# Optimization experiments

Measured on AMD Instinct MI355X. Metric: run time of the kernel, lower is better.

## Reference

```python
import jax, jax.numpy as jnp
import numpy as np

EMB = 768
NH = 12
DH = EMB // NH
NORM = float(np.sqrt(DH))  # 8.0


def setup_inputs() -> dict:
    key = jax.random.key(0)
    ks = jax.random.split(key, 9)
    B, S = 1, 4096
    s = 0.02  # realistic init scale for weights
    return {
        "x": jax.random.normal(ks[0], (B, S, EMB), jnp.float32),
        "mask": jnp.ones((B, S), jnp.float32),
        "Wq": jax.random.normal(ks[1], (EMB, EMB), jnp.float32) * s,
        "bq": jnp.zeros((EMB,), jnp.float32),
        "Wk": jax.random.normal(ks[2], (EMB, EMB), jnp.float32) * s,
        "bk": jnp.zeros((EMB,), jnp.float32),
        "Wv": jax.random.normal(ks[3], (EMB, EMB), jnp.float32) * s,
        "bv": jnp.zeros((EMB,), jnp.float32),
        "Wo": jax.random.normal(ks[4], (EMB, EMB), jnp.float32) * s,
        "bo": jnp.zeros((EMB,), jnp.float32),
    }


def reference(x, mask, Wq, bq, Wk, bk, Wv, bv, Wo, bo):
    B, S, _ = x.shape
    # QKV projections (torch Linear: x @ W.T + b)
    q = x @ Wq.T + bq
    k = x @ Wk.T + bk
    v = x @ Wv.T + bv
    # split heads: b s (nh dh) -> b nh s dh
    split = lambda t: t.reshape(B, S, NH, DH).transpose(0, 2, 1, 3)
    qh, kh, vh = split(q), split(k), split(v)
    # attention scores [b, nh, s, s]
    scores = jnp.einsum("bhqd,bhkd->bhqk", qh, kh) / NORM
    # additive mask: scores -= 10000 * (1 - mask), mask broadcast over query dim
    scores = scores - 10000.0 * (1.0 - mask[:, None, None, :])
    attn = jax.nn.softmax(scores, axis=-1)
    out = jnp.einsum("bhqk,bhkd->bhqd", attn, vh)
    # b nh s dh -> b s (nh dh)
    out = out.transpose(0, 2, 1, 3).reshape(B, S, EMB)
    return out @ Wo.T + bo
```

## Files before the change

kernel.cpp:

```cpp
#include <hip/hip_runtime.h>
#include <stdint.h>
#include <stddef.h>

#define EMB 768
#define SEQ 4096
#define NH 12
#define DH 64
#define LOG2E 1.44269504f
#define HALF (SEQ / 2)
#define NBLK (NH * 32 * 2)

typedef __attribute__((ext_vector_type(8))) short short8;
typedef __attribute__((ext_vector_type(2))) float f32x2;
typedef __attribute__((ext_vector_type(4))) float f32x4;
typedef __attribute__((ext_vector_type(8))) float f32x8;
typedef __attribute__((ext_vector_type(16))) float f32x16;
typedef __attribute__((ext_vector_type(2))) unsigned int uint32x2;

static __device__ __forceinline__ unsigned short f2bf(float f) {
  union { float f; uint32_t u; } v; v.f = f;
  uint32_t u = v.u;
  return (unsigned short)((u + 0x7FFFu + ((u >> 16) & 1u)) >> 16);
}

static __device__ __forceinline__ void gl_lds16(const void* g, void* l) {
  __builtin_amdgcn_global_load_lds(
      (const __attribute__((address_space(1))) uint32_t*)g,
      (__attribute__((address_space(3))) uint32_t*)l, 16, 0, 0);
}
static __device__ __forceinline__ void gl_lds4(const void* g, void* l) {
  __builtin_amdgcn_global_load_lds(
      (const __attribute__((address_space(1))) uint32_t*)g,
      (__attribute__((address_space(3))) uint32_t*)l, 4, 0, 0);
}

static __device__ __forceinline__ float xhalf_max(float v) {
  union { float f; unsigned int u; } x; x.f = v;
  uint32x2 r = __builtin_amdgcn_permlane32_swap(x.u, x.u, false, false);
  union { unsigned int u; float f; } a, b; a.u = r[0]; b.u = r[1];
  return fmaxf(a.f, b.f);
}
static __device__ __forceinline__ float xhalf_sum(float v) {
  union { float f; unsigned int u; } x; x.f = v;
  uint32x2 r = __builtin_amdgcn_permlane32_swap(x.u, x.u, false, false);
  union { unsigned int u; float f; } a, b; a.u = r[0]; b.u = r[1];
  return a.f + b.f;
}

static __device__ __forceinline__ f32x8 lo8(f32x16 v) {
  return __builtin_shufflevector(v, v, 0, 1, 2, 3, 4, 5, 6, 7);
}
static __device__ __forceinline__ f32x8 hi8(f32x16 v) {
  return __builtin_shufflevector(v, v, 8, 9, 10, 11, 12, 13, 14, 15);
}
static __device__ __forceinline__ f32x4 lo4(f32x8 v) {
  return __builtin_shufflevector(v, v, 0, 1, 2, 3);
}
static __device__ __forceinline__ f32x4 hi4(f32x8 v) {
  return __builtin_shufflevector(v, v, 4, 5, 6, 7);
}
static __device__ __forceinline__ f32x2 lo2(f32x4 v) {
  return __builtin_shufflevector(v, v, 0, 1);
}
static __device__ __forceinline__ f32x2 hi2(f32x4 v) {
  return __builtin_shufflevector(v, v, 2, 3);
}

__global__ void prep_kernel(const float* __restrict__ x, const float* __restrict__ mask,
                            const float* __restrict__ Wq, const float* __restrict__ Wk,
                            const float* __restrict__ Wv, const float* __restrict__ Wo,
                            unsigned short* __restrict__ xb, unsigned short* __restrict__ wqb,
                            unsigned short* __restrict__ wkb, unsigned short* __restrict__ wvb,
                            unsigned short* __restrict__ wob, float* __restrict__ mb2) {
  const int y = blockIdx.y;
  if (y == 5) {
    int i = blockIdx.x * 256 + threadIdx.x;
    if (i < SEQ) mb2[i] = -80000.f * (1.f - mask[i]);
    return;
  }
  const float* in = y == 0 ? x : y == 1 ? Wq : y == 2 ? Wk : y == 3 ? Wv : Wo;
  unsigned short* out = y == 0 ? xb : y == 1 ? wqb : y == 2 ? wkb : y == 3 ? wvb : wob;
  const int n = (y == 0) ? SEQ * EMB : EMB * EMB;
  int stride = gridDim.x * blockDim.x * 4;
  for (int i = (blockIdx.x * blockDim.x + threadIdx.x) * 4; i < n; i += stride) {
    float4 v = *reinterpret_cast<const float4*>(in + i);
    ushort4 o;
    o.x = f2bf(v.x); o.y = f2bf(v.y); o.z = f2bf(v.z); o.w = f2bf(v.w);
    *reinterpret_cast<ushort4*>(out + i) = o;
  }
}

template <int OUT_F32>
static __device__ __forceinline__ void gemm128(
    const unsigned short* __restrict__ A, const unsigned short* __restrict__ W,
    const float* __restrict__ bias, void* __restrict__ Cout,
    int M, int N, int K, int bm, int bn) {
  __shared__ unsigned short Alds[128 * 64];
  __shared__ unsigned short Blds[128 * 64];
  const int t = threadIdx.x;
  const int lane = t & 63;
  const int wave = t >> 6;
  const int wr = wave >> 1, wc = wave & 1;
  const int lm = lane & 15, lg = lane >> 4;

  f32x4 acc[4][4];
#pragma unroll
  for (int i = 0; i < 4; ++i)
#pragma unroll
    for (int j = 0; j < 4; ++j) acc[i][j] = (f32x4){0.f, 0.f, 0.f, 0.f};

  const int srow = t >> 3;
  const int scsw = (t & 7) * 16;

  const int nK = K >> 6;
  for (int kt = 0; kt < nK; ++kt) {
    const int k0 = kt << 6;
#pragma unroll
    for (int i = 0; i < 4; ++i) {
      int row = i * 32 + srow;
      int cb = scsw ^ ((row & 7) << 4);
      gl_lds16(A + (size_t)(bm * 128 + row) * K + k0 + (cb >> 1),
               (char*)Alds + i * 4096 + t * 16);
      gl_lds16(W + (size_t)(bn * 128 + row) * K + k0 + (cb >> 1),
               (char*)Blds + i * 4096 + t * 16);
    }
    __syncthreads();
#pragma unroll
    for (int kk = 0; kk < 2; ++kk) {
      short8 af[4], bfr[4];
#pragma unroll
      for (int i = 0; i < 4; ++i) {
        int rowa = wr * 64 + i * 16 + lm;
        int cba = (kk * 64 + lg * 16) ^ ((rowa & 7) << 4);
        af[i] = *reinterpret_cast<const short8*>((const char*)Alds + rowa * 128 + cba);
        int rowb = wc * 64 + i * 16 + lm;
        int cbb = (kk * 64 + lg * 16) ^ ((rowb & 7) << 4);
        bfr[i] = *reinterpret_cast<const short8*>((const char*)Blds + rowb * 128 + cbb);
      }
#pragma unroll
      for (int i = 0; i < 4; ++i)
#pragma unroll
        for (int j = 0; j < 4; ++j)
          acc[i][j] = __builtin_amdgcn_mfma_f32_16x16x32_bf16(af[i], bfr[j], acc[i][j], 0, 0, 0);
    }
    __syncthreads();
  }
#pragma unroll
  for (int i = 0; i < 4; ++i) {
    int row0 = bm * 128 + wr * 64 + i * 16 + lg * 4;
#pragma unroll
    for (int j = 0; j < 4; ++j) {
      int col = bn * 128 + wc * 64 + j * 16 + lm;
      float b = bias[col];
#pragma unroll
      for (int r = 0; r < 4; ++r) {
        float v = acc[i][j][r] + b;
        if (OUT_F32)
          ((float*)Cout)[(size_t)(row0 + r) * N + col] = v;
        else
          ((unsigned short*)Cout)[(size_t)(row0 + r) * N + col] = f2bf(v);
      }
    }
  }
}

__global__ __launch_bounds__(256, 2) void gemm_wo(
    const unsigned short* __restrict__ A, const unsigned short* __restrict__ W,
    const float* __restrict__ bias, float* __restrict__ C) {
  gemm128<1>(A, W, bias, C, SEQ, EMB, EMB, blockIdx.x, blockIdx.y);
}

__global__ __launch_bounds__(256, 2) void qkv_gemm(
    const unsigned short* __restrict__ A,
    const unsigned short* __restrict__ W0, const unsigned short* __restrict__ W1,
    const unsigned short* __restrict__ W2,
    const float* __restrict__ b0, const float* __restrict__ b1, const float* __restrict__ b2,
    unsigned short* __restrict__ O0, unsigned short* __restrict__ O1,
    unsigned short* __restrict__ O2) {
  const int z = blockIdx.z;
  const unsigned short* W = z == 0 ? W0 : z == 1 ? W1 : W2;
  const float* bias = z == 0 ? b0 : z == 1 ? b1 : b2;
  unsigned short* O = z == 0 ? O0 : z == 1 ? O1 : O2;
  gemm128<0>(A, W, bias, O, SEQ, EMB, EMB, blockIdx.x, blockIdx.y);
}

__global__ void transpose_kernel(const unsigned short* __restrict__ in,
                                 unsigned short* __restrict__ out) {
  __shared__ unsigned short tile[32][33];
  int tx = threadIdx.x, ty = threadIdx.y;
  int e0 = blockIdx.x * 32, s0 = blockIdx.y * 32;
#pragma unroll
  for (int i = 0; i < 4; ++i)
    tile[ty + i * 8][tx] = in[(size_t)(s0 + ty + i * 8) * EMB + e0 + tx];
  __syncthreads();
#pragma unroll
  for (int i = 0; i < 4; ++i)
    out[(size_t)(e0 + ty + i * 8) * SEQ + s0 + tx] = tile[tx][ty + i * 8];
}

__global__ __launch_bounds__(256, 3) void attn_kernel(
    const unsigned short* __restrict__ Q, const unsigned short* __restrict__ Kb,
    const unsigned short* __restrict__ Vt, const float* __restrict__ mb2,
    float* __restrict__ opart, float* __restrict__ mpart,
    float* __restrict__ lpart) {
  __shared__ unsigned short Klds[2][64 * DH];
  __shared__ unsigned short Vlds[2][DH * 64];
  __shared__ __align__(16) float msk[2][64];
  __shared__ __align__(16) float bcs[4][32];

  const int t = threadIdx.x;
  const int lane = t & 63;
  const int wave = t >> 6;
  const int o = blockIdx.x;
  const int wg = (o & 7) * (NBLK / 8) + (o >> 3);
  const int head = wg >> 6;
  const int rem = wg & 63;
  const int qb = rem >> 1;
  const int sp = rem & 1;
  const int q0 = qb * 128 + wave * 32;
  const int kvb0 = sp * HALF;
  const int lm = lane & 31;
  const int h = lane >> 5;

  short8 qf[4];
#pragma unroll
  for (int ks = 0; ks < 4; ++ks)
    qf[ks] = *reinterpret_cast<const short8*>(
        Q + (size_t)(q0 + lm) * EMB + head * DH + ks * 16 + h * 8);

  f32x16 oacc[2];
#pragma unroll
  for (int n = 0; n < 2; ++n)
#pragma unroll
    for (int r = 0; r < 16; ++r) oacc[n][r] = 0.f;
  float mrun = -3.0e38f, lrun = 0.f;

  const int srow = t >> 3;
  const int scol = (t & 7) * 16;

  auto STAGE = [&](int buf, int kt2) {
    const int kv0 = kvb0 + kt2 * 64;
#pragma unroll
    for (int i = 0; i < 2; ++i) {
      int row = i * 32 + srow;
      int cb = scol ^ ((row & 7) << 4);
      gl_lds16(Kb + (size_t)(kv0 + row) * EMB + head * DH + (cb >> 1),
               (char*)Klds + buf * 8192 + i * 4096 + t * 16);
      gl_lds16(Vt + (size_t)(head * DH + row) * SEQ + kv0 + (cb >> 1),
               (char*)Vlds + buf * 8192 + i * 4096 + t * 16);
    }
    gl_lds4(mb2 + kv0 + lane, &msk[buf][0]);
  };

  constexpr int NT = HALF / 64;
  STAGE(0, 0);
  __syncthreads();

  for (int kt = 0; kt < NT; ++kt) {
    const int buf = kt & 1;
    if (kt + 1 < NT) STAGE(buf ^ 1, kt + 1);

    f32x16 s[2];
#pragma unroll
    for (int tt = 0; tt < 2; ++tt)
#pragma unroll
      for (int a = 0; a < 4; ++a) {
        f32x4 m = *reinterpret_cast<const f32x4*>(&msk[buf][tt * 32 + a * 8 + h * 4]);
#pragma unroll
        for (int i = 0; i < 4; ++i) s[tt][a * 4 + i] = m[i];
      }

    __builtin_amdgcn_s_setprio(1);
#pragma unroll
    for (int tt = 0; tt < 2; ++tt)
#pragma unroll
      for (int ks = 0; ks < 4; ++ks) {
        int row = tt * 32 + lm;
        int cb = (ks * 32 + h * 16) ^ ((row & 7) << 4);
        short8 kf = *reinterpret_cast<const short8*>(
            (const char*)Klds + buf * 8192 + row * 128 + cb);
        s[tt] = __builtin_amdgcn_mfma_f32_32x32x16_bf16(kf, qf[ks], s[tt], 0, 0, 0);
      }
    __builtin_amdgcn_s_setprio(0);

    const float sc2 = 0.125f * LOG2E;
    s[0] = s[0] * sc2;
    s[1] = s[1] * sc2;

    f32x16 mx16 = __builtin_elementwise_max(s[0], s[1]);
    f32x8 mx8 = __builtin_elementwise_max(lo8(mx16), hi8(mx16));
    f32x4 mx4 = __builtin_elementwise_max(lo4(mx8), hi4(mx8));
    f32x2 mx2 = __builtin_elementwise_max(lo2(mx4), hi2(mx4));
    float pm = xhalf_max(fmaxf(mx2[0], mx2[1]));

    if (!__all(pm <= mrun + 8.0f)) {
      float mnew = fmaxf(mrun, pm);
      float sf = __builtin_amdgcn_exp2f(mrun - mnew);
      mrun = mnew;
      lrun *= sf;
      bcs[wave][lm] = sf;
      f32x16 svv;
#pragma unroll
      for (int a = 0; a < 4; ++a) {
        f32x4 sv = *reinterpret_cast<const f32x4*>(&bcs[wave][a * 8 + h * 4]);
#pragma unroll
        for (int i = 0; i < 4; ++i) svv[a * 4 + i] = sv[i];
      }
      oacc[0] = oacc[0] * svv;
      oacc[1] = oacc[1] * svv;
    }

    s[0] = s[0] - mrun;
    s[1] = s[1] - mrun;
#pragma unroll
    for (int tt = 0; tt < 2; ++tt)
#pragma unroll
      for (int r = 0; r < 16; ++r)
        s[tt][r] = __builtin_amdgcn_exp2f(s[tt][r]);

    f32x16 sm16 = s[0] + s[1];
    f32x8 sm8 = lo8(sm16) + hi8(sm16);
    f32x4 sm4 = lo4(sm8) + hi4(sm8);
    f32x2 sm2 = lo2(sm4) + hi2(sm4);
    lrun += xhalf_sum(sm2[0] + sm2[1]);

    short8 pa[4];
#pragma unroll
    for (int tt = 0; tt < 2; ++tt) {
      uint32_t r0[4], r1[4];
#pragma unroll
      for (int a = 0; a < 4; ++a) {
        asm("v_cvt_pk_bf16_f32 %0, %1, %2" : "=v"(r0[a]) : "v"(s[tt][4 * a]), "v"(s[tt][4 * a + 1]));
        asm("v_cvt_pk_bf16_f32 %0, %1, %2" : "=v"(r1[a]) : "v"(s[tt][4 * a + 2]), "v"(s[tt][4 * a + 3]));
      }
#pragma unroll
      for (int ksl = 0; ksl < 2; ++ksl) {
        uint32x2 w0 = __builtin_amdgcn_permlane32_swap(r0[2 * ksl], r0[2 * ksl + 1], false, false);
        uint32x2 w1 = __builtin_amdgcn_permlane32_swap(r1[2 * ksl], r1[2 * ksl + 1], false, false);
        union { short8 s8; uint32_t u[4]; } pk;
        pk.u[0] = w0[0]; pk.u[1] = w1[0]; pk.u[2] = w0[1]; pk.u[3] = w1[1];
        pa[tt * 2 + ksl] = pk.s8;
      }
    }

    __builtin_amdgcn_s_setprio(1);
#pragma unroll
    for (int n = 0; n < 2; ++n)
#pragma unroll
      for (int ks = 0; ks < 4; ++ks) {
        int row = n * 32 + lm;
        int cb = (ks * 32 + h * 16) ^ ((row & 7) << 4);
        short8 vf = *reinterpret_cast<const short8*>(
            (const char*)Vlds + buf * 8192 + row * 128 + cb);
        oacc[n] = __builtin_amdgcn_mfma_f32_32x32x16_bf16(pa[ks], vf, oacc[n], 0, 0, 0);
      }
    __builtin_amdgcn_s_setprio(0);

    __syncthreads();
  }

  float* ob = opart + ((size_t)(sp * NH + head) * SEQ + q0) * 64;
#pragma unroll
  for (int n = 0; n < 2; ++n)
#pragma unroll
    for (int r = 0; r < 16; ++r) {
      int crow = (r & 3) + 8 * (r >> 2) + 4 * h;
      ob[crow * 64 + n * 32 + lm] = oacc[n][r];
    }
  if (h == 0) {
    mpart[(size_t)(sp * NH + head) * SEQ + q0 + lm] = mrun;
    lpart[(size_t)(sp * NH + head) * SEQ + q0 + lm] = lrun;
  }
}

__global__ void merge_kernel(const float* __restrict__ opart,
                             const float* __restrict__ mpart,
                             const float* __restrict__ lpart,
                             unsigned short* __restrict__ Ab) {
  int tid = blockIdx.x * 256 + threadIdx.x;
  int dv = tid & 15;
  int rq = tid >> 4;
  int head = rq >> 12;
  int q = rq & 4095;
  size_t i0 = (size_t)head * SEQ + q;
  size_t i1 = (size_t)(NH + head) * SEQ + q;
  float m0 = mpart[i0], m1 = mpart[i1];
  float l0 = lpart[i0], l1 = lpart[i1];
  float m = fmaxf(m0, m1);
  float w0 = __builtin_amdgcn_exp2f(m0 - m);
  float w1 = __builtin_amdgcn_exp2f(m1 - m);
  float rl = 1.0f / fmaf(w0, l0, w1 * l1);
  f32x4 o0 = *reinterpret_cast<const f32x4*>(opart + i0 * 64 + dv * 4);
  f32x4 o1 = *reinterpret_cast<const f32x4*>(opart + i1 * 64 + dv * 4);
  ushort4 r;
  r.x = f2bf((o0[0] * w0 + o1[0] * w1) * rl);
  r.y = f2bf((o0[1] * w0 + o1[1] * w1) * rl);
  r.z = f2bf((o0[2] * w0 + o1[2] * w1) * rl);
  r.w = f2bf((o0[3] * w0 + o1[3] * w1) * rl);
  *reinterpret_cast<ushort4*>(Ab + (size_t)q * EMB + head * DH + dv * 4) = r;
}

extern "C" void kernel_launch(void* const* d_in, const int* in_sizes, int n_in,
                              void* d_out, int out_size, void* d_ws, size_t ws_size,
                              hipStream_t stream) {
  const float* x    = (const float*)d_in[0];
  const float* mask = (const float*)d_in[1];
  const float* Wq   = (const float*)d_in[2];
  const float* bq   = (const float*)d_in[3];
  const float* Wk   = (const float*)d_in[4];
  const float* bk   = (const float*)d_in[5];
  const float* Wv   = (const float*)d_in[6];
  const float* bv   = (const float*)d_in[7];
  const float* Wo   = (const float*)d_in[8];
  const float* bo   = (const float*)d_in[9];
  float* out = (float*)d_out;

  char* ws = (char*)d_ws;
  const size_t SZ_X = (size_t)SEQ * EMB * 2;
  const size_t SZ_W = (size_t)EMB * EMB * 2;
  unsigned short* xb  = (unsigned short*)(ws);
  unsigned short* wqb = (unsigned short*)(ws + SZ_X);
  unsigned short* wkb = (unsigned short*)(ws + SZ_X + SZ_W);
  unsigned short* wvb = (unsigned short*)(ws + SZ_X + 2 * SZ_W);
  unsigned short* wob = (unsigned short*)(ws + SZ_X + 3 * SZ_W);
  unsigned short* Qb  = (unsigned short*)(ws + SZ_X + 4 * SZ_W);
  unsigned short* Kbuf= (unsigned short*)(ws + 2 * SZ_X + 4 * SZ_W);
  unsigned short* Vb  = (unsigned short*)(ws + 3 * SZ_X + 4 * SZ_W);
  unsigned short* Vtb = (unsigned short*)(ws + 4 * SZ_X + 4 * SZ_W);
  unsigned short* Ab  = (unsigned short*)(ws + 5 * SZ_X + 4 * SZ_W);
  size_t off = 6 * SZ_X + 4 * SZ_W;
  float* mb2   = (float*)(ws + off);              off += (size_t)SEQ * 4;
  float* opart = (float*)(ws + off);              off += (size_t)2 * NH * SEQ * 64 * 4;
  float* mpart = (float*)(ws + off);              off += (size_t)2 * NH * SEQ * 4;
  float* lpart = (float*)(ws + off);

  prep_kernel<<<dim3(192, 6), 256, 0, stream>>>(
      x, mask, Wq, Wk, Wv, Wo, xb, wqb, wkb, wvb, wob, mb2);

  qkv_gemm<<<dim3(SEQ / 128, EMB / 128, 3), 256, 0, stream>>>(
      xb, wqb, wkb, wvb, bq, bk, bv, Qb, Kbuf, Vb);

  transpose_kernel<<<dim3(EMB / 32, SEQ / 32), dim3(32, 8), 0, stream>>>(Vb, Vtb);

  attn_kernel<<<NBLK, 256, 0, stream>>>(Qb, Kbuf, Vtb, mb2, opart, mpart, lpart);
  merge_kernel<<<3072, 256, 0, stream>>>(opart, mpart, lpart, Ab);

  gemm_wo<<<dim3(SEQ / 128, EMB / 128), 256, 0, stream>>>(Ab, wob, bo, out);
}
```

Before: 132.0 us.

## Split attention KV into four chunks with 32-key tiles and bf16 normalized partials

The attention kernel now splits each query block's keys across four workgroups instead of two, and shrinks the per-iteration KV tile from 64 to 32 keys. This halves LDS use and raises the occupancy hint to 6 blocks per CU. Partial outputs are normalized by the running sum in the kernel and stored as bf16 rather than fp32, which cuts partial-result traffic. The merge kernel combines four partials weighted by exp(m)*l. In exchange, each tile does less work per sync, the merge does more total work, and the bf16 partials add rounding error.

Result: slower. 168.2 us (+27.4%).

```diff
diff --git a/kernel.cpp b/kernel.cpp
--- a/kernel.cpp
+++ b/kernel.cpp
@@ -7,13 +7,13 @@
 #define NH 12
 #define DH 64
 #define LOG2E 1.44269504f
-#define HALF (SEQ / 2)
-#define NBLK (NH * 32 * 2)
+#define NSP 4
+#define SPLEN (SEQ / NSP)
+#define KVB 32
+#define NBLK (NH * 32 * NSP)
 
 typedef __attribute__((ext_vector_type(8))) short short8;
-typedef __attribute__((ext_vector_type(2))) float f32x2;
 typedef __attribute__((ext_vector_type(4))) float f32x4;
-typedef __attribute__((ext_vector_type(8))) float f32x8;
 typedef __attribute__((ext_vector_type(16))) float f32x16;
 typedef __attribute__((ext_vector_type(2))) unsigned int uint32x2;
 
@@ -21,6 +21,10 @@
   union { float f; uint32_t u; } v; v.f = f;
   uint32_t u = v.u;
   return (unsigned short)((u + 0x7FFFu + ((u >> 16) & 1u)) >> 16);
+}
+static __device__ __forceinline__ float bf2f(unsigned short s) {
+  union { uint32_t u; float f; } v; v.u = ((uint32_t)s) << 16;
+  return v.f;
 }
 
 static __device__ __forceinline__ void gl_lds16(const void* g, void* l) {
@@ -45,25 +49,6 @@
   uint32x2 r = __builtin_amdgcn_permlane32_swap(x.u, x.u, false, false);
   union { unsigned int u; float f; } a, b; a.u = r[0]; b.u = r[1];
   return a.f + b.f;
-}
-
-static __device__ __forceinline__ f32x8 lo8(f32x16 v) {
-  return __builtin_shufflevector(v, v, 0, 1, 2, 3, 4, 5, 6, 7);
-}
-static __device__ __forceinline__ f32x8 hi8(f32x16 v) {
-  return __builtin_shufflevector(v, v, 8, 9, 10, 11, 12, 13, 14, 15);
-}
-static __device__ __forceinline__ f32x4 lo4(f32x8 v) {
-  return __builtin_shufflevector(v, v, 0, 1, 2, 3);
-}
-static __device__ __forceinline__ f32x4 hi4(f32x8 v) {
-  return __builtin_shufflevector(v, v, 4, 5, 6, 7);
-}
-static __device__ __forceinline__ f32x2 lo2(f32x4 v) {
-  return __builtin_shufflevector(v, v, 0, 1);
-}
-static __device__ __forceinline__ f32x2 hi2(f32x4 v) {
-  return __builtin_shufflevector(v, v, 2, 3);
 }
 
 __global__ void prep_kernel(const float* __restrict__ x, const float* __restrict__ mask,
@@ -198,14 +183,14 @@
     out[(size_t)(e0 + ty + i * 8) * SEQ + s0 + tx] = tile[tx][ty + i * 8];
 }
 
-__global__ __launch_bounds__(256, 3) void attn_kernel(
+__global__ __launch_bounds__(256, 6) void attn_kernel(
     const unsigned short* __restrict__ Q, const unsigned short* __restrict__ Kb,
     const unsigned short* __restrict__ Vt, const float* __restrict__ mb2,
-    float* __restrict__ opart, float* __restrict__ mpart,
+    unsigned short* __restrict__ opart, float* __restrict__ mpart,
     float* __restrict__ lpart) {
-  __shared__ unsigned short Klds[2][64 * DH];
-  __shared__ unsigned short Vlds[2][DH * 64];
-  __shared__ __align__(16) float msk[2][64];
+  __shared__ unsigned short Klds[2][KVB * DH];
+  __shared__ unsigned short Vlds[2][KVB * DH];
+  __shared__ __align__(16) float msk[2][KVB];
   __shared__ __align__(16) float bcs[4][32];
 
   const int t = threadIdx.x;
@@ -213,12 +198,12 @@
   const int wave = t >> 6;
   const int o = blockIdx.x;
   const int wg = (o & 7) * (NBLK / 8) + (o >> 3);
-  const int head = wg >> 6;
-  const int rem = wg & 63;
-  const int qb = rem >> 1;
-  const int sp = rem & 1;
+  const int head = wg >> 7;
+  const int rem = wg & 127;
+  const int qb = rem >> 2;
+  const int sp = rem & 3;
   const int q0 = qb * 128 + wave * 32;
-  const int kvb0 = sp * HALF;
+  const int kvb0 = sp * SPLEN;
   const int lm = lane & 31;
   const int h = lane >> 5;
 
@@ -236,23 +221,21 @@
   float mrun = -3.0e38f, lrun = 0.f;
 
   const int srow = t >> 3;
-  const int scol = (t & 7) * 16;
+  const int so16 = t & 7;
 
   auto STAGE = [&](int buf, int kt2) {
-    const int kv0 = kvb0 + kt2 * 64;
-#pragma unroll
-    for (int i = 0; i < 2; ++i) {
-      int row = i * 32 + srow;
-      int cb = scol ^ ((row & 7) << 4);
-      gl_lds16(Kb + (size_t)(kv0 + row) * EMB + head * DH + (cb >> 1),
-               (char*)Klds + buf * 8192 + i * 4096 + t * 16);
-      gl_lds16(Vt + (size_t)(head * DH + row) * SEQ + kv0 + (cb >> 1),
-               (char*)Vlds + buf * 8192 + i * 4096 + t * 16);
-    }
-    gl_lds4(mb2 + kv0 + lane, &msk[buf][0]);
+    const int kv0 = kvb0 + kt2 * KVB;
+    int kcb = (so16 * 16) ^ ((srow & 7) << 4);
+    gl_lds16(Kb + (size_t)(kv0 + srow) * EMB + head * DH + (kcb >> 1),
+             (char*)Klds + buf * 4096 + t * 16);
+    int vo16p = so16 ^ (srow & 7);
+    int vd = 2 * srow + (vo16p >> 2);
+    gl_lds16(Vt + (size_t)(head * DH + vd) * SEQ + kv0 + (vo16p & 3) * 8,
+             (char*)Vlds + buf * 4096 + t * 16);
+    if (lane < KVB) gl_lds4(mb2 + kv0 + lane, &msk[buf][0]);
   };
 
-  constexpr int NT = HALF / 64;
+  constexpr int NT = SPLEN / KVB;
   STAGE(0, 0);
   __syncthreads();
 
@@ -260,38 +243,36 @@
     const int buf = kt & 1;
     if (kt + 1 < NT) STAGE(buf ^ 1, kt + 1);
 
-    f32x16 s[2];
-#pragma unroll
-    for (int tt = 0; tt < 2; ++tt)
-#pragma unroll
-      for (int a = 0; a < 4; ++a) {
-        f32x4 m = *reinterpret_cast<const f32x4*>(&msk[buf][tt * 32 + a * 8 + h * 4]);
-#pragma unroll
-        for (int i = 0; i < 4; ++i) s[tt][a * 4 + i] = m[i];
-      }
+    f32x16 s;
+#pragma unroll
+    for (int a = 0; a < 4; ++a) {
+      f32x4 m = *reinterpret_cast<const f32x4*>(&msk[buf][a * 8 + h * 4]);
+#pragma unroll
+      for (int i = 0; i < 4; ++i) s[a * 4 + i] = m[i];
+    }
 
     __builtin_amdgcn_s_setprio(1);
 #pragma unroll
-    for (int tt = 0; tt < 2; ++tt)
-#pragma unroll
-      for (int ks = 0; ks < 4; ++ks) {
-        int row = tt * 32 + lm;
-        int cb = (ks * 32 + h * 16) ^ ((row & 7) << 4);
-        short8 kf = *reinterpret_cast<const short8*>(
-            (const char*)Klds + buf * 8192 + row * 128 + cb);
-        s[tt] = __builtin_amdgcn_mfma_f32_32x32x16_bf16(kf, qf[ks], s[tt], 0, 0, 0);
-      }
+    for (int ks = 0; ks < 4; ++ks) {
+      int cb = (ks * 32 + h * 16) ^ ((lm & 7) << 4);
+      short8 kf = *reinterpret_cast<const short8*>(
+          (const char*)Klds + buf * 4096 + lm * 128 + cb);
+      s = __builtin_amdgcn_mfma_f32_32x32x16_bf16(kf, qf[ks], s, 0, 0, 0);
+    }
     __builtin_amdgcn_s_setprio(0);
 
     const float sc2 = 0.125f * LOG2E;
-    s[0] = s[0] * sc2;
-    s[1] = s[1] * sc2;
-
-    f32x16 mx16 = __builtin_elementwise_max(s[0], s[1]);
-    f32x8 mx8 = __builtin_elementwise_max(lo8(mx16), hi8(mx16));
-    f32x4 mx4 = __builtin_elementwise_max(lo4(mx8), hi4(mx8));
-    f32x2 mx2 = __builtin_elementwise_max(lo2(mx4), hi2(mx4));
-    float pm = xhalf_max(fmaxf(mx2[0], mx2[1]));
+#pragma unroll
+    for (int r = 0; r < 16; ++r) s[r] *= sc2;
+
+    float red[8];
+#pragma unroll
+    for (int r = 0; r < 8; ++r) red[r] = fmaxf(s[r], s[r + 8]);
+#pragma unroll
+    for (int off = 4; off >= 1; off >>= 1)
+#pragma unroll
+      for (int r = 0; r < off; ++r) red[r] = fmaxf(red[r], red[r + off]);
+    float pm = xhalf_max(red[0]);
 
     if (!__all(pm <= mrun + 8.0f)) {
       float mnew = fmaxf(mrun, pm);
@@ -310,48 +291,46 @@
       oacc[1] = oacc[1] * svv;
     }
 
-    s[0] = s[0] - mrun;
-    s[1] = s[1] - mrun;
-#pragma unroll
-    for (int tt = 0; tt < 2; ++tt)
-#pragma unroll
-      for (int r = 0; r < 16; ++r)
-        s[tt][r] = __builtin_amdgcn_exp2f(s[tt][r]);
-
-    f32x16 sm16 = s[0] + s[1];
-    f32x8 sm8 = lo8(sm16) + hi8(sm16);
-    f32x4 sm4 = lo4(sm8) + hi4(sm8);
-    f32x2 sm2 = lo2(sm4) + hi2(sm4);
-    lrun += xhalf_sum(sm2[0] + sm2[1]);
-
-    short8 pa[4];
-#pragma unroll
-    for (int tt = 0; tt < 2; ++tt) {
-      uint32_t r0[4], r1[4];
-#pragma unroll
-      for (int a = 0; a < 4; ++a) {
-        asm("v_cvt_pk_bf16_f32 %0, %1, %2" : "=v"(r0[a]) : "v"(s[tt][4 * a]), "v"(s[tt][4 * a + 1]));
-        asm("v_cvt_pk_bf16_f32 %0, %1, %2" : "=v"(r1[a]) : "v"(s[tt][4 * a + 2]), "v"(s[tt][4 * a + 3]));
-      }
-#pragma unroll
-      for (int ksl = 0; ksl < 2; ++ksl) {
-        uint32x2 w0 = __builtin_amdgcn_permlane32_swap(r0[2 * ksl], r0[2 * ksl + 1], false, false);
-        uint32x2 w1 = __builtin_amdgcn_permlane32_swap(r1[2 * ksl], r1[2 * ksl + 1], false, false);
-        union { short8 s8; uint32_t u[4]; } pk;
-        pk.u[0] = w0[0]; pk.u[1] = w1[0]; pk.u[2] = w0[1]; pk.u[3] = w1[1];
-        pa[tt * 2 + ksl] = pk.s8;
-      }
+#pragma unroll
+    for (int r = 0; r < 16; ++r)
+      s[r] = __builtin_amdgcn_exp2f(s[r] - mrun);
+
+    float rs[8];
+#pragma unroll
+    for (int r = 0; r < 8; ++r) rs[r] = s[r] + s[r + 8];
+#pragma unroll
+    for (int off = 4; off >= 1; off >>= 1)
+#pragma unroll
+      for (int r = 0; r < off; ++r) rs[r] += rs[r + off];
+    lrun += xhalf_sum(rs[0]);
+
+    uint32_t r0[4], r1[4];
+#pragma unroll
+    for (int a = 0; a < 4; ++a) {
+      asm("v_cvt_pk_bf16_f32 %0, %1, %2" : "=v"(r0[a]) : "v"(s[4 * a]), "v"(s[4 * a + 1]));
+      asm("v_cvt_pk_bf16_f32 %0, %1, %2" : "=v"(r1[a]) : "v"(s[4 * a + 2]), "v"(s[4 * a + 3]));
+    }
+    short8 pa[2];
+#pragma unroll
+    for (int ksl = 0; ksl < 2; ++ksl) {
+      uint32x2 w0 = __builtin_amdgcn_permlane32_swap(r0[2 * ksl], r0[2 * ksl + 1], false, false);
+      uint32x2 w1 = __builtin_amdgcn_permlane32_swap(r1[2 * ksl], r1[2 * ksl + 1], false, false);
+      union { short8 s8; uint32_t u[4]; } pk;
+      pk.u[0] = w0[0]; pk.u[1] = w1[0]; pk.u[2] = w0[1]; pk.u[3] = w1[1];
+      pa[ksl] = pk.s8;
     }
 
     __builtin_amdgcn_s_setprio(1);
 #pragma unroll
     for (int n = 0; n < 2; ++n)
 #pragma unroll
-      for (int ks = 0; ks < 4; ++ks) {
-        int row = n * 32 + lm;
-        int cb = (ks * 32 + h * 16) ^ ((row & 7) << 4);
+      for (int ks = 0; ks < 2; ++ks) {
+        int d = n * 32 + lm;
+        int row = d >> 1;
+        int o16p = (d & 1) * 4 + ks * 2 + h;
+        int cb = ((o16p ^ (row & 7)) << 4);
         short8 vf = *reinterpret_cast<const short8*>(
-            (const char*)Vlds + buf * 8192 + row * 128 + cb);
+            (const char*)Vlds + buf * 4096 + row * 128 + cb);
         oacc[n] = __builtin_amdgcn_mfma_f32_32x32x16_bf16(pa[ks], vf, oacc[n], 0, 0, 0);
       }
     __builtin_amdgcn_s_setprio(0);
@@ -359,13 +338,21 @@
     __syncthreads();
   }
 
-  float* ob = opart + ((size_t)(sp * NH + head) * SEQ + q0) * 64;
+  bcs[wave][lm] = __builtin_amdgcn_rcpf(lrun);
+  f32x16 lv;
+#pragma unroll
+  for (int a = 0; a < 4; ++a) {
+    f32x4 sv = *reinterpret_cast<const f32x4*>(&bcs[wave][a * 8 + h * 4]);
+#pragma unroll
+    for (int i = 0; i < 4; ++i) lv[a * 4 + i] = sv[i];
+  }
+  unsigned short* ob = opart + ((size_t)(sp * NH + head) * SEQ + q0) * 64;
 #pragma unroll
   for (int n = 0; n < 2; ++n)
 #pragma unroll
     for (int r = 0; r < 16; ++r) {
       int crow = (r & 3) + 8 * (r >> 2) + 4 * h;
-      ob[crow * 64 + n * 32 + lm] = oacc[n][r];
+      ob[crow * 64 + n * 32 + lm] = f2bf(oacc[n][r] * lv[r]);
     }
   if (h == 0) {
     mpart[(size_t)(sp * NH + head) * SEQ + q0 + lm] = mrun;
@@ -373,7 +360,7 @@
   }
 }
 
-__global__ void merge_kernel(const float* __restrict__ opart,
+__global__ void merge_kernel(const unsigned short* __restrict__ opart,
                              const float* __restrict__ mpart,
                              const float* __restrict__ lpart,
                              unsigned short* __restrict__ Ab) {
@@ -382,21 +369,37 @@
   int rq = tid >> 4;
   int head = rq >> 12;
   int q = rq & 4095;
-  size_t i0 = (size_t)head * SEQ + q;
-  size_t i1 = (size_t)(NH + head) * SEQ + q;
-  float m0 = mpart[i0], m1 = mpart[i1];
-  float l0 = lpart[i0], l1 = lpart[i1];
-  float m = fmaxf(m0, m1);
-  float w0 = __builtin_amdgcn_exp2f(m0 - m);
-  float w1 = __builtin_amdgcn_exp2f(m1 - m);
-  float rl = 1.0f / fmaf(w0, l0, w1 * l1);
-  f32x4 o0 = *reinterpret_cast<const f32x4*>(opart + i0 * 64 + dv * 4);
-  f32x4 o1 = *reinterpret_cast<const f32x4*>(opart + i1 * 64 + dv * 4);
+  size_t base = (size_t)head * SEQ + q;
+  const size_t str = (size_t)NH * SEQ;
+
+  float m[NSP], l[NSP];
+#pragma unroll
+  for (int sp = 0; sp < NSP; ++sp) {
+    m[sp] = mpart[base + sp * str];
+    l[sp] = lpart[base + sp * str];
+  }
+  float mx = fmaxf(fmaxf(m[0], m[1]), fmaxf(m[2], m[3]));
+  float w[NSP], denom = 0.f;
+#pragma unroll
+  for (int sp = 0; sp < NSP; ++sp) {
+    w[sp] = __builtin_amdgcn_exp2f(m[sp] - mx) * l[sp];
+    denom += w[sp];
+  }
+  float rd = 1.0f / denom;
+
+  float acc0 = 0.f, acc1 = 0.f, acc2 = 0.f, acc3 = 0.f;
+#pragma unroll
+  for (int sp = 0; sp < NSP; ++sp) {
+    float c = w[sp] * rd;
+    ushort4 ov = *reinterpret_cast<const ushort4*>(
+        opart + (base + sp * str) * 64 + dv * 4);
+    acc0 += c * bf2f(ov.x);
+    acc1 += c * bf2f(ov.y);
+    acc2 += c * bf2f(ov.z);
+    acc3 += c * bf2f(ov.w);
+  }
   ushort4 r;
-  r.x = f2bf((o0[0] * w0 + o1[0] * w1) * rl);
-  r.y = f2bf((o0[1] * w0 + o1[1] * w1) * rl);
-  r.z = f2bf((o0[2] * w0 + o1[2] * w1) * rl);
-  r.w = f2bf((o0[3] * w0 + o1[3] * w1) * rl);
+  r.x = f2bf(acc0); r.y = f2bf(acc1); r.z = f2bf(acc2); r.w = f2bf(acc3);
   *reinterpret_cast<ushort4*>(Ab + (size_t)q * EMB + head * DH + dv * 4) = r;
 }
 
@@ -429,10 +432,10 @@
   unsigned short* Vtb = (unsigned short*)(ws + 4 * SZ_X + 4 * SZ_W);
   unsigned short* Ab  = (unsigned short*)(ws + 5 * SZ_X + 4 * SZ_W);
   size_t off = 6 * SZ_X + 4 * SZ_W;
-  float* mb2   = (float*)(ws + off);              off += (size_t)SEQ * 4;
-  float* opart = (float*)(ws + off);              off += (size_t)2 * NH * SEQ * 64 * 4;
-  float* mpart = (float*)(ws + off);              off += (size_t)2 * NH * SEQ * 4;
-  float* lpart = (float*)(ws + off);
+  float* mb2            = (float*)(ws + off);          off += (size_t)SEQ * 4;
+  unsigned short* opart = (unsigned short*)(ws + off); off += (size_t)NSP * NH * SEQ * 64 * 2;
+  float* mpart          = (float*)(ws + off);          off += (size_t)NSP * NH * SEQ * 4;
+  float* lpart          = (float*)(ws + off);
 
   prep_kernel<<<dim3(192, 6), 256, 0, stream>>>(
       x, mask, Wq, Wk, Wv, Wo, xb, wqb, wkb, wvb, wob, mb2);
```

## Compute softmax row sums via MFMA, fold scale into exp, store bf16 partials

Applied to the files above, without the earlier changes.

Replaces the per-tile VALU row-sum reduction with an extra MFMA against a ones vector, so the accumulated row sums land in the same layout as the output accumulator. The scale multiply and max subtraction are folded into a single fma inside exp2, and the max reduction runs on unscaled scores. Partial outputs are normalized in the attention kernel and written as bf16, which halves the partial-output traffic and simplifies the merge kernel. The cost is four extra MFMAs per tile and some extra precision loss from rounding the partials to bf16.

After: 127.7 us. 1.03x faster.

```diff
diff --git a/kernel.cpp b/kernel.cpp
--- a/kernel.cpp
+++ b/kernel.cpp
@@ -7,13 +7,12 @@
 #define NH 12
 #define DH 64
 #define LOG2E 1.44269504f
-#define HALF (SEQ / 2)
-#define NBLK (NH * 32 * 2)
+#define NSP 2
+#define SPLEN (SEQ / NSP)
+#define NBLK (NH * 32 * NSP)
 
 typedef __attribute__((ext_vector_type(8))) short short8;
-typedef __attribute__((ext_vector_type(2))) float f32x2;
 typedef __attribute__((ext_vector_type(4))) float f32x4;
-typedef __attribute__((ext_vector_type(8))) float f32x8;
 typedef __attribute__((ext_vector_type(16))) float f32x16;
 typedef __attribute__((ext_vector_type(2))) unsigned int uint32x2;
 
@@ -21,6 +20,10 @@
   union { float f; uint32_t u; } v; v.f = f;
   uint32_t u = v.u;
   return (unsigned short)((u + 0x7FFFu + ((u >> 16) & 1u)) >> 16);
+}
+static __device__ __forceinline__ float bf2f(unsigned short s) {
+  union { uint32_t u; float f; } v; v.u = ((uint32_t)s) << 16;
+  return v.f;
 }
 
 static __device__ __forceinline__ void gl_lds16(const void* g, void* l) {
@@ -39,31 +42,6 @@
   uint32x2 r = __builtin_amdgcn_permlane32_swap(x.u, x.u, false, false);
   union { unsigned int u; float f; } a, b; a.u = r[0]; b.u = r[1];
   return fmaxf(a.f, b.f);
-}
-static __device__ __forceinline__ float xhalf_sum(float v) {
-  union { float f; unsigned int u; } x; x.f = v;
-  uint32x2 r = __builtin_amdgcn_permlane32_swap(x.u, x.u, false, false);
-  union { unsigned int u; float f; } a, b; a.u = r[0]; b.u = r[1];
-  return a.f + b.f;
-}
-
-static __device__ __forceinline__ f32x8 lo8(f32x16 v) {
-  return __builtin_shufflevector(v, v, 0, 1, 2, 3, 4, 5, 6, 7);
-}
-static __device__ __forceinline__ f32x8 hi8(f32x16 v) {
-  return __builtin_shufflevector(v, v, 8, 9, 10, 11, 12, 13, 14, 15);
-}
-static __device__ __forceinline__ f32x4 lo4(f32x8 v) {
-  return __builtin_shufflevector(v, v, 0, 1, 2, 3);
-}
-static __device__ __forceinline__ f32x4 hi4(f32x8 v) {
-  return __builtin_shufflevector(v, v, 4, 5, 6, 7);
-}
-static __device__ __forceinline__ f32x2 lo2(f32x4 v) {
-  return __builtin_shufflevector(v, v, 0, 1);
-}
-static __device__ __forceinline__ f32x2 hi2(f32x4 v) {
-  return __builtin_shufflevector(v, v, 2, 3);
 }
 
 __global__ void prep_kernel(const float* __restrict__ x, const float* __restrict__ mask,
@@ -201,7 +179,7 @@
 __global__ __launch_bounds__(256, 3) void attn_kernel(
     const unsigned short* __restrict__ Q, const unsigned short* __restrict__ Kb,
     const unsigned short* __restrict__ Vt, const float* __restrict__ mb2,
-    float* __restrict__ opart, float* __restrict__ mpart,
+    unsigned short* __restrict__ opart, float* __restrict__ mpart,
     float* __restrict__ lpart) {
   __shared__ unsigned short Klds[2][64 * DH];
   __shared__ unsigned short Vlds[2][DH * 64];
@@ -218,7 +196,7 @@
   const int qb = rem >> 1;
   const int sp = rem & 1;
   const int q0 = qb * 128 + wave * 32;
-  const int kvb0 = sp * HALF;
+  const int kvb0 = sp * SPLEN;
   const int lm = lane & 31;
   const int h = lane >> 5;
 
@@ -228,12 +206,18 @@
     qf[ks] = *reinterpret_cast<const short8*>(
         Q + (size_t)(q0 + lm) * EMB + head * DH + ks * 16 + h * 8);
 
-  f32x16 oacc[2];
+  short8 ones;
+#pragma unroll
+  for (int i = 0; i < 8; ++i) ones[i] = (short)0x3F80;
+
+  f32x16 oacc[2], lacc;
 #pragma unroll
   for (int n = 0; n < 2; ++n)
 #pragma unroll
     for (int r = 0; r < 16; ++r) oacc[n][r] = 0.f;
-  float mrun = -3.0e38f, lrun = 0.f;
+#pragma unroll
+  for (int r = 0; r < 16; ++r) lacc[r] = 0.f;
+  float mrun = -3.0e38f;
 
   const int srow = t >> 3;
   const int scol = (t & 7) * 16;
@@ -252,9 +236,11 @@
     gl_lds4(mb2 + kv0 + lane, &msk[buf][0]);
   };
 
-  constexpr int NT = HALF / 64;
+  constexpr int NT = SPLEN / 64;
   STAGE(0, 0);
   __syncthreads();
+
+  const float sc2 = 0.125f * LOG2E;
 
   for (int kt = 0; kt < NT; ++kt) {
     const int buf = kt & 1;
@@ -283,21 +269,24 @@
       }
     __builtin_amdgcn_s_setprio(0);
 
-    const float sc2 = 0.125f * LOG2E;
-    s[0] = s[0] * sc2;
-    s[1] = s[1] * sc2;
-
-    f32x16 mx16 = __builtin_elementwise_max(s[0], s[1]);
-    f32x8 mx8 = __builtin_elementwise_max(lo8(mx16), hi8(mx16));
-    f32x4 mx4 = __builtin_elementwise_max(lo4(mx8), hi4(mx8));
-    f32x2 mx2 = __builtin_elementwise_max(lo2(mx4), hi2(mx4));
-    float pm = xhalf_max(fmaxf(mx2[0], mx2[1]));
+    float red[8];
+#pragma unroll
+    for (int r = 0; r < 8; ++r)
+      red[r] = fmaxf(fmaxf(s[0][r], s[0][r + 8]), s[1][r]);
+#pragma unroll
+    for (int r = 0; r < 4; ++r)
+      red[r] = fmaxf(fmaxf(red[r], red[r + 4]), s[1][8 + r]);
+#pragma unroll
+    for (int r = 0; r < 2; ++r)
+      red[r] = fmaxf(fmaxf(red[r], red[r + 2]), s[1][12 + r]);
+    red[0] = fmaxf(fmaxf(red[0], red[1]), s[1][14]);
+    red[0] = fmaxf(red[0], s[1][15]);
+    float pm = xhalf_max(red[0]) * sc2;
 
     if (!__all(pm <= mrun + 8.0f)) {
       float mnew = fmaxf(mrun, pm);
       float sf = __builtin_amdgcn_exp2f(mrun - mnew);
       mrun = mnew;
-      lrun *= sf;
       bcs[wave][lm] = sf;
       f32x16 svv;
 #pragma unroll
@@ -308,21 +297,14 @@
       }
       oacc[0] = oacc[0] * svv;
       oacc[1] = oacc[1] * svv;
-    }
-
-    s[0] = s[0] - mrun;
-    s[1] = s[1] - mrun;
+      lacc = lacc * svv;
+    }
+
 #pragma unroll
     for (int tt = 0; tt < 2; ++tt)
 #pragma unroll
       for (int r = 0; r < 16; ++r)
-        s[tt][r] = __builtin_amdgcn_exp2f(s[tt][r]);
-
-    f32x16 sm16 = s[0] + s[1];
-    f32x8 sm8 = lo8(sm16) + hi8(sm16);
-    f32x4 sm4 = lo4(sm8) + hi4(sm8);
-    f32x2 sm2 = lo2(sm4) + hi2(sm4);
-    lrun += xhalf_sum(sm2[0] + sm2[1]);
+        s[tt][r] = __builtin_amdgcn_exp2f(fmaf(s[tt][r], sc2, -mrun));
 
     short8 pa[4];
 #pragma unroll
@@ -354,26 +336,37 @@
             (const char*)Vlds + buf * 8192 + row * 128 + cb);
         oacc[n] = __builtin_amdgcn_mfma_f32_32x32x16_bf16(pa[ks], vf, oacc[n], 0, 0, 0);
       }
+#pragma unroll
+    for (int ks = 0; ks < 4; ++ks)
+      lacc = __builtin_amdgcn_mfma_f32_32x32x16_bf16(pa[ks], ones, lacc, 0, 0, 0);
     __builtin_amdgcn_s_setprio(0);
 
     __syncthreads();
   }
 
-  float* ob = opart + ((size_t)(sp * NH + head) * SEQ + q0) * 64;
+  f32x16 rl;
+#pragma unroll
+  for (int r = 0; r < 16; ++r) rl[r] = __builtin_amdgcn_rcpf(lacc[r]);
+  unsigned short* ob = opart + ((size_t)(sp * NH + head) * SEQ + q0) * 64;
 #pragma unroll
   for (int n = 0; n < 2; ++n)
 #pragma unroll
     for (int r = 0; r < 16; ++r) {
       int crow = (r & 3) + 8 * (r >> 2) + 4 * h;
-      ob[crow * 64 + n * 32 + lm] = oacc[n][r];
-    }
-  if (h == 0) {
-    mpart[(size_t)(sp * NH + head) * SEQ + q0 + lm] = mrun;
-    lpart[(size_t)(sp * NH + head) * SEQ + q0 + lm] = lrun;
-  }
-}
-
-__global__ void merge_kernel(const float* __restrict__ opart,
+      ob[crow * 64 + n * 32 + lm] = f2bf(oacc[n][r] * rl[r]);
+    }
+  const size_t pbase = (size_t)(sp * NH + head) * SEQ + q0;
+  if (h == 0) mpart[pbase + lm] = mrun;
+  if (lm == 0) {
+#pragma unroll
+    for (int r = 0; r < 16; ++r) {
+      int crow = (r & 3) + 8 * (r >> 2) + 4 * h;
+      lpart[pbase + crow] = lacc[r];
+    }
+  }
+}
+
+__global__ void merge_kernel(const unsigned short* __restrict__ opart,
                              const float* __restrict__ mpart,
                              const float* __restrict__ lpart,
                              unsigned short* __restrict__ Ab) {
@@ -382,21 +375,24 @@
   int rq = tid >> 4;
   int head = rq >> 12;
   int q = rq & 4095;
-  size_t i0 = (size_t)head * SEQ + q;
-  size_t i1 = (size_t)(NH + head) * SEQ + q;
-  float m0 = mpart[i0], m1 = mpart[i1];
-  float l0 = lpart[i0], l1 = lpart[i1];
-  float m = fmaxf(m0, m1);
-  float w0 = __builtin_amdgcn_exp2f(m0 - m);
-  float w1 = __builtin_amdgcn_exp2f(m1 - m);
-  float rl = 1.0f / fmaf(w0, l0, w1 * l1);
-  f32x4 o0 = *reinterpret_cast<const f32x4*>(opart + i0 * 64 + dv * 4);
-  f32x4 o1 = *reinterpret_cast<const f32x4*>(opart + i1 * 64 + dv * 4);
+  size_t base = (size_t)head * SEQ + q;
+  const size_t str = (size_t)NH * SEQ;
+
+  float m0 = mpart[base], m1 = mpart[base + str];
+  float l0 = lpart[base], l1 = lpart[base + str];
+  float mx = fmaxf(m0, m1);
+  float w0 = __builtin_amdgcn_exp2f(m0 - mx) * l0;
+  float w1 = __builtin_amdgcn_exp2f(m1 - mx) * l1;
+  float rd = 1.0f / (w0 + w1);
+  float c0 = w0 * rd, c1 = w1 * rd;
+
+  ushort4 o0 = *reinterpret_cast<const ushort4*>(opart + base * 64 + dv * 4);
+  ushort4 o1 = *reinterpret_cast<const ushort4*>(opart + (base + str) * 64 + dv * 4);
   ushort4 r;
-  r.x = f2bf((o0[0] * w0 + o1[0] * w1) * rl);
-  r.y = f2bf((o0[1] * w0 + o1[1] * w1) * rl);
-  r.z = f2bf((o0[2] * w0 + o1[2] * w1) * rl);
-  r.w = f2bf((o0[3] * w0 + o1[3] * w1) * rl);
+  r.x = f2bf(c0 * bf2f(o0.x) + c1 * bf2f(o1.x));
+  r.y = f2bf(c0 * bf2f(o0.y) + c1 * bf2f(o1.y));
+  r.z = f2bf(c0 * bf2f(o0.z) + c1 * bf2f(o1.z));
+  r.w = f2bf(c0 * bf2f(o0.w) + c1 * bf2f(o1.w));
   *reinterpret_cast<ushort4*>(Ab + (size_t)q * EMB + head * DH + dv * 4) = r;
 }
 
@@ -429,10 +425,10 @@
   unsigned short* Vtb = (unsigned short*)(ws + 4 * SZ_X + 4 * SZ_W);
   unsigned short* Ab  = (unsigned short*)(ws + 5 * SZ_X + 4 * SZ_W);
   size_t off = 6 * SZ_X + 4 * SZ_W;
-  float* mb2   = (float*)(ws + off);              off += (size_t)SEQ * 4;
-  float* opart = (float*)(ws + off);              off += (size_t)2 * NH * SEQ * 64 * 4;
-  float* mpart = (float*)(ws + off);              off += (size_t)2 * NH * SEQ * 4;
-  float* lpart = (float*)(ws + off);
+  float* mb2            = (float*)(ws + off);          off += (size_t)SEQ * 4;
+  unsigned short* opart = (unsigned short*)(ws + off); off += (size_t)NSP * NH * SEQ * 64 * 2;
+  float* mpart          = (float*)(ws + off);          off += (size_t)NSP * NH * SEQ * 4;
+  float* lpart          = (float*)(ws + off);
 
   prep_kernel<<<dim3(192, 6), 256, 0, stream>>>(
       x, mask, Wq, Wk, Wv, Wo, xb, wqb, wkb, wvb, wob, mb2);
```
